# Kernel tuning notes

Hardware: AMD Instinct MI355X
Metric: run time of the kernel (lower is better)

Reference implementation:

```python
import jax, jax.numpy as jnp
import numpy as np

C_IN, C_OUT, K = 4, 8, 5


def _causal_conv1d(x, w):
    # x: [B, c_in, S]; reflection-pad left by K-1, VALID conv -> [B, c_out, S]
    xp = jnp.pad(x, ((0, 0), (0, 0), (K - 1, 0)), mode='reflect')
    return jax.lax.conv_general_dilated(
        xp, w, window_strides=(1,), padding='VALID',
        dimension_numbers=('NCH', 'OIH', 'NCH'))


def setup_inputs() -> dict:
    key = jax.random.key(0)
    ks = jax.random.split(key, 8)
    B, S = 16, 2048
    q = jax.random.normal(ks[0], (B, C_IN, S), dtype=jnp.float32)
    k = jax.random.normal(ks[1], (B, C_IN, S), dtype=jnp.float32)
    v = jax.random.normal(ks[2], (B, C_IN, S), dtype=jnp.float32)
    scale = 1.0 / np.sqrt(C_IN * K)
    wq = jax.random.normal(ks[3], (C_OUT, C_IN, K), dtype=jnp.float32) * scale
    wk = jax.random.normal(ks[4], (C_OUT, C_IN, K), dtype=jnp.float32) * scale
    wv = jax.random.normal(ks[5], (C_OUT, C_IN, K), dtype=jnp.float32) * scale
    w_out = jax.random.normal(ks[6], (C_OUT, C_OUT), dtype=jnp.float32) * (1.0 / np.sqrt(C_OUT))
    b_out = jax.random.normal(ks[7], (C_OUT,), dtype=jnp.float32) * 0.01
    return {"q": q, "k": k, "v": v, "wq": wq, "wk": wk, "wv": wv,
            "w_out": w_out, "b_out": b_out}


def reference(q, k, v, wq, wk, wv, w_out, b_out):
    # Conv-derived embeddings. NOTE: source wires v_conv(k) and k_conv(v).
    qe = _causal_conv1d(q, wq)   # [B, c_out, S]
    ve = _causal_conv1d(k, wv)   # v_conv applied to k (as in source)
    ke = _causal_conv1d(v, wk)   # k_conv applied to v (as in source)
    d_k = C_OUT                  # self.h == c_out
    # scores: contract over channel dim -> [B, S, S]
    scores = jnp.einsum('bcs,bct->bst', qe, ke) / jnp.sqrt(jnp.asarray(d_k, qe.dtype))
    attn = jax.nn.softmax(scores, axis=-1)
    # attn @ v^T -> [B, S, c_out]
    out = jnp.einsum('bst,bct->bsc', attn, ve)
    out = out @ w_out.T + b_out  # Linear(c_out, c_out)
    return jnp.swapaxes(out, -1, -2)  # [B, c_out, S]
```

## Files before the change

kernel.cpp:

```cpp
#include <hip/hip_runtime.h>

#define B 16
#define CIN 4
#define COUT 8
#define KW 5
#define S 2048
#define BS (B * S)

typedef _Float16 f16;
typedef _Float16 f16x4 __attribute__((ext_vector_type(4)));
typedef _Float16 f16x8 __attribute__((ext_vector_type(8)));
typedef __fp16 fp16x2 __attribute__((ext_vector_type(2)));
typedef float f32x16 __attribute__((ext_vector_type(16)));

__device__ __forceinline__ int vfrag_off(int k) {
    return (((k >> 2) & 1) << 4) | (((k >> 4) & 1) << 3) | (k & 3) | (((k >> 3) & 1) << 2);
}

__global__ __launch_bounds__(256) void conv_embed_kernel(
    const float* __restrict__ q, const float* __restrict__ k,
    const float* __restrict__ v, const float* __restrict__ wq,
    const float* __restrict__ wk, const float* __restrict__ wv,
    f16* __restrict__ qe, f16* __restrict__ ke, f16* __restrict__ vt2)
{
    __shared__ float wsm[80];

    int tid  = threadIdx.x;
    int bid  = blockIdx.x;
    int xcd  = bid & 7;
    int slot = bid >> 3;
    int grp  = slot >> 4;
    int r    = slot & 15;
    int b    = xcd + ((r >> 3) << 3);
    int chunk= r & 7;
    int part = grp >> 1;
    int oh   = grp & 1;

    const float* in; const float* wsrc;
    if (part == 0)      { in = q; wsrc = wq; }
    else if (part == 1) { in = v; wsrc = wk; }
    else                { in = k; wsrc = wv; }

    if (tid < 80) wsm[tid] = wsrc[oh * 80 + tid];
    __syncthreads();

    int s = chunk * 256 + tid;
    int gid = b * S + s;

    float x[CIN][KW];
#pragma unroll
    for (int c = 0; c < CIN; ++c) {
        const float* ip = in + ((size_t)(b * CIN + c) << 11);
#pragma unroll
        for (int i = 0; i < KW; ++i) {
            int idx = s + i - 4;
            idx = idx < 0 ? -idx : idx;
            x[c][i] = ip[idx];
        }
    }

    float o[4];
#pragma unroll
    for (int oo = 0; oo < 4; ++oo) {
        float a = 0.f;
#pragma unroll
        for (int c = 0; c < CIN; ++c)
#pragma unroll
            for (int i = 0; i < KW; ++i)
                a += x[c][i] * wsm[oo * 20 + c * 5 + i];
        o[oo] = a;
    }

    const float QSCALE = 0.35355339059327373f * 1.4426950408889634f;

    if (part == 2) {
        int t   = s >> 5;
        int off = vfrag_off(s & 31);
        size_t base = (size_t)(b * 64 + t) * 9;
#pragma unroll
        for (int oo = 0; oo < 4; ++oo)
            vt2[((base + oh * 4 + oo) << 5) + off] = (f16)o[oo];
        if (oh == 0)
            vt2[((base + 8) << 5) + off] = (f16)1.0f;
    } else {
        float sc = (part == 0) ? QSCALE : 1.0f;
        f16x4 r4;
#pragma unroll
        for (int oo = 0; oo < 4; ++oo) r4[oo] = (f16)(o[oo] * sc);
        f16* dst = ((part == 0) ? qe : ke) + ((size_t)gid << 3) + oh * 4;
        *(f16x4*)dst = r4;
    }
}

#define QT 32
#define NWAVE 8
#define KVC (S / NWAVE)

#if __has_builtin(__builtin_amdgcn_mfma_f32_32x32x8f16)
#define HAVE_K8 1
#else
#define HAVE_K8 0
#endif

__global__ __launch_bounds__(512, 4) void attn_mfma_kernel(
    const f16* __restrict__ qe, const f16* __restrict__ ke,
    const f16* __restrict__ vt2, const float* __restrict__ w_out,
    const float* __restrict__ b_out, float* __restrict__ out)
{
    __shared__ float red[NWAVE][9][QT];

    int tid  = threadIdx.x;
    int w    = tid >> 6;
    int lane = tid & 63;
    int hi   = lane >> 5;
    int ln   = lane & 31;

    int bid  = blockIdx.x;
    int xcd  = bid & 7;
    int slot = bid >> 3;
    int b    = xcd + ((slot >> 6) << 3);
    int q0   = (slot & 63) * QT;

    f16x4 qb4 = *(const f16x4*)(qe + ((size_t)(b * S + q0 + ln) << 3) + hi * 4);
#if !HAVE_K8
    f16x8 qb8 = {qb4[0], qb4[1], qb4[2], qb4[3], (f16)0, (f16)0, (f16)0, (f16)0};
#endif

    const f32x16 zero16 = {};
    f32x16 oacc = {};

    int vrow = ln < 9 ? ln : 8;
    const f16* kptr = ke + ((size_t)(b * S + w * KVC + ln) << 3) + hi * 4;
    const f16* vptr = vt2 + (((size_t)(b * 64 + w * (KVC / 32)) * 9 + vrow) << 5) + hi * 16;

#pragma unroll
    for (int it = 0; it < KVC / 32; ++it) {
        f16x4 kh = *(const f16x4*)kptr;
        kptr += 32 * 8;
#if HAVE_K8
        f32x16 sc = __builtin_amdgcn_mfma_f32_32x32x8f16(kh, qb4, zero16, 0, 0, 0);
#else
        f16x8 ka = {kh[0], kh[1], kh[2], kh[3], (f16)0, (f16)0, (f16)0, (f16)0};
        f32x16 sc = __builtin_amdgcn_mfma_f32_32x32x16_f16(ka, qb8, zero16, 0, 0, 0);
#endif

        union { f16x8 v; fp16x2 h[4]; } p1, p2;
#pragma unroll
        for (int i = 0; i < 4; ++i) {
            p1.h[i] = __builtin_amdgcn_cvt_pkrtz(__builtin_amdgcn_exp2f(sc[2 * i]),
                                                 __builtin_amdgcn_exp2f(sc[2 * i + 1]));
            p2.h[i] = __builtin_amdgcn_cvt_pkrtz(__builtin_amdgcn_exp2f(sc[8 + 2 * i]),
                                                 __builtin_amdgcn_exp2f(sc[8 + 2 * i + 1]));
        }

        f16x8 va1 = *(const f16x8*)(vptr);
        f16x8 va2 = *(const f16x8*)(vptr + 8);
        vptr += 9 * 32;

        oacc = __builtin_amdgcn_mfma_f32_32x32x16_f16(va1, p1.v, oacc, 0, 0, 0);
        oacc = __builtin_amdgcn_mfma_f32_32x32x16_f16(va2, p2.v, oacc, 0, 0, 0);
    }

#pragma unroll
    for (int r = 0; r < 16; ++r) {
        int n = (r & 3) + 8 * (r >> 2) + 4 * hi;
        if (n < 9) red[w][n][ln] = oacc[r];
    }
    __syncthreads();

    if (tid < 9 * QT) {
        int n = tid >> 5, qq = tid & 31;
        float a = red[0][n][qq];
#pragma unroll
        for (int ww = 1; ww < NWAVE; ++ww) a += red[ww][n][qq];
        red[0][n][qq] = a;
    }
    __syncthreads();

    if (tid < 256) {
        int cp = tid >> 5, qq = tid & 31;
        float inv = 1.0f / red[0][8][qq];
        float y = b_out[cp];
#pragma unroll
        for (int c = 0; c < 8; ++c) y += w_out[cp * 8 + c] * red[0][c][qq] * inv;
        out[(((size_t)(b * COUT + cp)) << 11) + q0 + qq] = y;
    }
}

extern "C" void kernel_launch(void* const* d_in, const int* in_sizes, int n_in,
                              void* d_out, int out_size, void* d_ws, size_t ws_size,
                              hipStream_t stream)
{
    const float* q     = (const float*)d_in[0];
    const float* k     = (const float*)d_in[1];
    const float* v     = (const float*)d_in[2];
    const float* wq    = (const float*)d_in[3];
    const float* wk    = (const float*)d_in[4];
    const float* wv    = (const float*)d_in[5];
    const float* w_out = (const float*)d_in[6];
    const float* b_out = (const float*)d_in[7];
    float* out = (float*)d_out;

    f16* qe  = (f16*)d_ws;
    f16* ke  = qe + (size_t)BS * COUT;
    f16* vt2 = ke + (size_t)BS * COUT;

    conv_embed_kernel<<<768, 256, 0, stream>>>(q, k, v, wq, wk, wv, qe, ke, vt2);
    attn_mfma_kernel<<<B * (S / QT), 512, 0, stream>>>(qe, ke, vt2, w_out, b_out, out);
}
```

Measured before the change: 18.62 us.

## Stage K/V tiles in shared memory and process two query tiles per block

Each attention block now handles two 32-query tiles instead of one, halving the grid. K and V fragments for each half of the sequence are cooperatively loaded into XOR-swizzled LDS once, and every wave reuses them for both query tiles. The goal is to halve global/L2 traffic for K and V and amortize the loads. In exchange it adds LDS usage, extra barriers, and doubled accumulator registers (launch bounds lowered to 2 blocks), with fewer blocks available to fill the GPU.

```diff
diff --git a/kernel.cpp b/kernel.cpp
--- a/kernel.cpp
+++ b/kernel.cpp
@@ -94,7 +94,6 @@
 
 #define QT 32
 #define NWAVE 8
-#define KVC (S / NWAVE)
 
 #if __has_builtin(__builtin_amdgcn_mfma_f32_32x32x8f16)
 #define HAVE_K8 1
@@ -102,11 +101,13 @@
 #define HAVE_K8 0
 #endif
 
-__global__ __launch_bounds__(512, 4) void attn_mfma_kernel(
+__global__ __launch_bounds__(512, 2) void attn_mfma_kernel(
     const f16* __restrict__ qe, const f16* __restrict__ ke,
     const f16* __restrict__ vt2, const float* __restrict__ w_out,
     const float* __restrict__ b_out, float* __restrict__ out)
 {
+    __shared__ f16 kls[1024 * 8];
+    __shared__ f16 vls[32 * 320];
     __shared__ float red[NWAVE][9][QT];
 
     int tid  = threadIdx.x;
@@ -118,72 +119,107 @@
     int bid  = blockIdx.x;
     int xcd  = bid & 7;
     int slot = bid >> 3;
-    int b    = xcd + ((slot >> 6) << 3);
-    int q0   = (slot & 63) * QT;
-
-    f16x4 qb4 = *(const f16x4*)(qe + ((size_t)(b * S + q0 + ln) << 3) + hi * 4);
+    int b    = xcd + ((slot >> 5) << 3);
+    int blks = slot & 31;
+
+    f16x4 qb[2];
+#pragma unroll
+    for (int qt = 0; qt < 2; ++qt) {
+        int q0 = (blks * 2 + qt) * QT;
+        qb[qt] = *(const f16x4*)(qe + ((size_t)(b * S + q0 + ln) << 3) + hi * 4);
+    }
 #if !HAVE_K8
-    f16x8 qb8 = {qb4[0], qb4[1], qb4[2], qb4[3], (f16)0, (f16)0, (f16)0, (f16)0};
+    f16x8 qb8[2];
+#pragma unroll
+    for (int qt = 0; qt < 2; ++qt)
+        qb8[qt] = (f16x8){qb[qt][0], qb[qt][1], qb[qt][2], qb[qt][3],
+                          (f16)0, (f16)0, (f16)0, (f16)0};
 #endif
 
     const f32x16 zero16 = {};
-    f32x16 oacc = {};
+    f32x16 oacc0 = {}, oacc1 = {};
 
     int vrow = ln < 9 ? ln : 8;
-    const f16* kptr = ke + ((size_t)(b * S + w * KVC + ln) << 3) + hi * 4;
-    const f16* vptr = vt2 + (((size_t)(b * 64 + w * (KVC / 32)) * 9 + vrow) << 5) + hi * 16;
-
-#pragma unroll
-    for (int it = 0; it < KVC / 32; ++it) {
-        f16x4 kh = *(const f16x4*)kptr;
-        kptr += 32 * 8;
+
+#pragma unroll
+    for (int h = 0; h < 2; ++h) {
+        __syncthreads();
+        for (int u = tid; u < 1024; u += 512) {
+            *(f16x8*)&kls[(u * 8) ^ (((u >> 3) & 1) << 3)] =
+                *(const f16x8*)(ke + ((size_t)(b * S + h * 1024 + u) << 3));
+        }
+        for (int u = tid; u < 1152; u += 512) {
+            int t = u / 36, r2 = u % 36, row = r2 >> 2, q4 = r2 & 3;
+            *(f16x8*)&vls[(t * 320 + row * 32 + q4 * 8) ^ (((row >> 1) & 3) << 4)] =
+                *(const f16x8*)(vt2 + ((((size_t)(b * 64 + h * 32 + t) * 9 + row) << 5) + q4 * 8));
+        }
+        __syncthreads();
+
+#pragma unroll
+        for (int it = 0; it < 4; ++it) {
+            int kvl = w * 128 + it * 32 + ln;
+            f16x4 kh = *(const f16x4*)&kls[((kvl * 8) ^ (((kvl >> 3) & 1) << 3)) + hi * 4];
+            int tl = w * 4 + it;
+            int voff = (tl * 320 + vrow * 32 + hi * 16) ^ (((vrow >> 1) & 3) << 4);
+            f16x8 va1 = *(const f16x8*)&vls[voff];
+            f16x8 va2 = *(const f16x8*)&vls[voff + 8];
+
+#pragma unroll
+            for (int qt = 0; qt < 2; ++qt) {
 #if HAVE_K8
-        f32x16 sc = __builtin_amdgcn_mfma_f32_32x32x8f16(kh, qb4, zero16, 0, 0, 0);
+                f32x16 sc = __builtin_amdgcn_mfma_f32_32x32x8f16(kh, qb[qt], zero16, 0, 0, 0);
 #else
-        f16x8 ka = {kh[0], kh[1], kh[2], kh[3], (f16)0, (f16)0, (f16)0, (f16)0};
-        f32x16 sc = __builtin_amdgcn_mfma_f32_32x32x16_f16(ka, qb8, zero16, 0, 0, 0);
+                f16x8 ka = {kh[0], kh[1], kh[2], kh[3], (f16)0, (f16)0, (f16)0, (f16)0};
+                f32x16 sc = __builtin_amdgcn_mfma_f32_32x32x16_f16(ka, qb8[qt], zero16, 0, 0, 0);
 #endif
-
-        union { f16x8 v; fp16x2 h[4]; } p1, p2;
-#pragma unroll
-        for (int i = 0; i < 4; ++i) {
-            p1.h[i] = __builtin_amdgcn_cvt_pkrtz(__builtin_amdgcn_exp2f(sc[2 * i]),
-                                                 __builtin_amdgcn_exp2f(sc[2 * i + 1]));
-            p2.h[i] = __builtin_amdgcn_cvt_pkrtz(__builtin_amdgcn_exp2f(sc[8 + 2 * i]),
-                                                 __builtin_amdgcn_exp2f(sc[8 + 2 * i + 1]));
-        }
-
-        f16x8 va1 = *(const f16x8*)(vptr);
-        f16x8 va2 = *(const f16x8*)(vptr + 8);
-        vptr += 9 * 32;
-
-        oacc = __builtin_amdgcn_mfma_f32_32x32x16_f16(va1, p1.v, oacc, 0, 0, 0);
-        oacc = __builtin_amdgcn_mfma_f32_32x32x16_f16(va2, p2.v, oacc, 0, 0, 0);
-    }
-
-#pragma unroll
-    for (int r = 0; r < 16; ++r) {
-        int n = (r & 3) + 8 * (r >> 2) + 4 * hi;
-        if (n < 9) red[w][n][ln] = oacc[r];
-    }
-    __syncthreads();
-
-    if (tid < 9 * QT) {
-        int n = tid >> 5, qq = tid & 31;
-        float a = red[0][n][qq];
-#pragma unroll
-        for (int ww = 1; ww < NWAVE; ++ww) a += red[ww][n][qq];
-        red[0][n][qq] = a;
-    }
-    __syncthreads();
-
-    if (tid < 256) {
-        int cp = tid >> 5, qq = tid & 31;
-        float inv = 1.0f / red[0][8][qq];
-        float y = b_out[cp];
-#pragma unroll
-        for (int c = 0; c < 8; ++c) y += w_out[cp * 8 + c] * red[0][c][qq] * inv;
-        out[(((size_t)(b * COUT + cp)) << 11) + q0 + qq] = y;
+                union { f16x8 v; fp16x2 h2[4]; } p1, p2;
+#pragma unroll
+                for (int i = 0; i < 4; ++i) {
+                    p1.h2[i] = __builtin_amdgcn_cvt_pkrtz(__builtin_amdgcn_exp2f(sc[2 * i]),
+                                                          __builtin_amdgcn_exp2f(sc[2 * i + 1]));
+                    p2.h2[i] = __builtin_amdgcn_cvt_pkrtz(__builtin_amdgcn_exp2f(sc[8 + 2 * i]),
+                                                          __builtin_amdgcn_exp2f(sc[8 + 2 * i + 1]));
+                }
+                if (qt == 0) {
+                    oacc0 = __builtin_amdgcn_mfma_f32_32x32x16_f16(va1, p1.v, oacc0, 0, 0, 0);
+                    oacc0 = __builtin_amdgcn_mfma_f32_32x32x16_f16(va2, p2.v, oacc0, 0, 0, 0);
+                } else {
+                    oacc1 = __builtin_amdgcn_mfma_f32_32x32x16_f16(va1, p1.v, oacc1, 0, 0, 0);
+                    oacc1 = __builtin_amdgcn_mfma_f32_32x32x16_f16(va2, p2.v, oacc1, 0, 0, 0);
+                }
+            }
+        }
+    }
+
+#pragma unroll
+    for (int qt = 0; qt < 2; ++qt) {
+        f32x16 oacc = (qt == 0) ? oacc0 : oacc1;
+        __syncthreads();
+#pragma unroll
+        for (int r = 0; r < 16; ++r) {
+            int n = (r & 3) + 8 * (r >> 2) + 4 * hi;
+            if (n < 9) red[w][n][ln] = oacc[r];
+        }
+        __syncthreads();
+
+        if (tid < 9 * QT) {
+            int n = tid >> 5, qq = tid & 31;
+            float a = red[0][n][qq];
+#pragma unroll
+            for (int ww = 1; ww < NWAVE; ++ww) a += red[ww][n][qq];
+            red[0][n][qq] = a;
+        }
+        __syncthreads();
+
+        if (tid < 256) {
+            int cp = tid >> 5, qq = tid & 31;
+            int q0 = (blks * 2 + qt) * QT;
+            float inv = 1.0f / red[0][8][qq];
+            float y = b_out[cp];
+#pragma unroll
+            for (int c = 0; c < 8; ++c) y += w_out[cp * 8 + c] * red[0][c][qq] * inv;
+            out[(((size_t)(b * COUT + cp)) << 11) + q0 + qq] = y;
+        }
     }
 }
 
@@ -206,5 +242,5 @@
     f16* vt2 = ke + (size_t)BS * COUT;
 
     conv_embed_kernel<<<768, 256, 0, stream>>>(q, k, v, wq, wk, wv, qe, ke, vt2);
-    attn_mfma_kernel<<<B * (S / QT), 512, 0, stream>>>(qe, ke, vt2, w_out, b_out, out);
-}
+    attn_mfma_kernel<<<512, 512, 0, stream>>>(qe, ke, vt2, w_out, b_out, out);
+}
```

Measured after the change: 19.69 us. 1.06x slower.
